# Kernel tuning notes

Measured on AMD Instinct MI355X. Metric: run time of the kernel, lower is better.

The kernel has to match this reference:

```python
import jax, jax.numpy as jnp
import numpy as np

BN_EPS = 1e-5


def spmm(rows, cols, vals, x):
    # Sparse [V,V] @ x for x: [B, V, F]. COO (rows, cols, vals) with E nnz.
    B, V, F = x.shape
    xt = jnp.transpose(x, (1, 0, 2)).reshape(V, B * F)      # [V, B*F]
    msg = xt[cols] * vals[:, None]                           # [E, B*F]
    y = jax.ops.segment_sum(msg, rows, num_segments=V)       # [V, B*F]
    return jnp.transpose(y.reshape(V, B, F), (1, 0, 2))      # [B, V, F]


def cheb_conv(rows, cols, vals, x, W, b):
    # Chebyshev graph conv: out = sum_k T_k(L) x @ W[k] + b ; W: [K, Fin, Fout]
    K = W.shape[0]
    x0 = x
    out = jnp.einsum('bvi,io->bvo', x0, W[0])
    if K > 1:
        x1 = spmm(rows, cols, vals, x0)
        out = out + jnp.einsum('bvi,io->bvo', x1, W[1])
        for k in range(2, K):
            x2 = 2.0 * spmm(rows, cols, vals, x1) - x0
            out = out + jnp.einsum('bvi,io->bvo', x2, W[k])
            x0, x1 = x1, x2
    return out + b


def bn_relu(x, gamma, beta):
    # BatchNorm1d (training stats) over (batch, nodes) per channel, then ReLU.
    m = jnp.mean(x, axis=(0, 1))
    v = jnp.var(x, axis=(0, 1))
    y = (x - m) * jax.lax.rsqrt(v + BN_EPS) * gamma + beta
    return jax.nn.relu(y)


def setup_inputs() -> dict:
    key = jax.random.key(0)
    ks = jax.random.split(key, 8)
    V, DEG, B, CIN, COUT = 49152, 20, 2, 128, 64
    x = jax.random.normal(ks[0], (B, V, CIN), dtype=jnp.float32)
    # HEALPix-like sparse Laplacian: diagonal + 20 random neighbors per node
    self_idx = jnp.arange(V, dtype=jnp.int32)
    nbr = jax.random.randint(ks[1], (V * DEG,), 0, V, dtype=jnp.int32)
    rows = jnp.concatenate([self_idx, jnp.repeat(self_idx, DEG)])
    cols = jnp.concatenate([self_idx, nbr])
    vals = jax.random.normal(ks[2], (V * (DEG + 1),), dtype=jnp.float32) * 0.1
    def w(k, shape):
        fan_in = shape[0] * shape[1]
        return jax.random.normal(k, shape, dtype=jnp.float32) * np.float32(np.sqrt(2.0 / fan_in))
    return {
        'x': x, 'rows': rows, 'cols': cols, 'vals': vals,
        'W1': w(ks[3], (1, CIN, COUT)), 'b1': jnp.zeros((COUT,), jnp.float32),
        'g1': jnp.ones((COUT,), jnp.float32), 'be1': jnp.zeros((COUT,), jnp.float32),
        'W2': w(ks[4], (3, COUT, COUT)), 'b2': jnp.zeros((COUT,), jnp.float32),
        'g2': jnp.ones((COUT,), jnp.float32), 'be2': jnp.zeros((COUT,), jnp.float32),
        'W3': w(ks[5], (1, COUT, CIN)), 'b3': jnp.zeros((CIN,), jnp.float32),
        'g3': jnp.ones((CIN,), jnp.float32), 'be3': jnp.zeros((CIN,), jnp.float32),
    }


def reference(x, rows, cols, vals, W1, b1, g1, be1, W2, b2, g2, be2, W3, b3, g3, be3):
    h = bn_relu(cheb_conv(rows, cols, vals, x, W1, b1), g1, be1)   # [B,V,64]
    h = bn_relu(cheb_conv(rows, cols, vals, h, W2, b2), g2, be2)   # [B,V,64]
    h = bn_relu(cheb_conv(rows, cols, vals, h, W3, b3), g3, be3)   # [B,V,128]
    return h
```

## Files before the change

### kernel.cpp

```cpp
#include <hip/hip_runtime.h>

#define VN 49152
#define DEG 20
#define NB 2
#define MROWS (NB * VN)

static constexpr float BN_EPS = 1e-5f;

typedef short bf16x8 __attribute__((ext_vector_type(8)));
typedef float floatx4 __attribute__((ext_vector_type(4)));

__device__ __forceinline__ unsigned short f2bf(float f) {
  unsigned int u = __builtin_bit_cast(unsigned int, f);
  u += 0x7FFFu + ((u >> 16) & 1u);
  return (unsigned short)(u >> 16);
}
__device__ __forceinline__ float bf2f(unsigned short h) {
  unsigned int u = ((unsigned int)h) << 16;
  return __builtin_bit_cast(float, u);
}
__device__ __forceinline__ float bflo(unsigned int u) {
  return __builtin_bit_cast(float, u << 16);
}
__device__ __forceinline__ float bfhi(unsigned int u) {
  return __builtin_bit_cast(float, u & 0xFFFF0000u);
}
__device__ __forceinline__ unsigned int packbf(float a, float b) {
  return (unsigned int)f2bf(a) | ((unsigned int)f2bf(b) << 16);
}


#define LDA1 136
__global__ __launch_bounds__(256) void gemm1(const float* __restrict__ X,
    const float* __restrict__ W, const float* __restrict__ bias,
    unsigned short* __restrict__ Y, float* __restrict__ st) {
  __shared__ unsigned short As[128 * LDA1];
  __shared__ unsigned short Bs[64 * LDA1];
  __shared__ float sred[128];
  int t = threadIdx.x;
  int row0 = blockIdx.x * 128;
  if (t < 128) sred[t] = 0.f;
  const float* Xt = X + (size_t)row0 * 128;
  #pragma unroll
  for (int c = 0; c < 16; ++c) {
    int f4i = c * 256 + t;
    int row = f4i >> 5, k = (f4i & 31) * 4;
    float4 v = *(const float4*)(Xt + row * 128 + k);
    *(uint2*)(&As[row * LDA1 + k]) = make_uint2(packbf(v.x, v.y), packbf(v.z, v.w));
  }
  #pragma unroll
  for (int c = 0; c < 32; ++c) {
    int f = c * 256 + t;
    int k = f >> 6, n = f & 63;
    Bs[n * LDA1 + k] = f2bf(W[f]);
  }
  __syncthreads();
  int l = t & 63, wv = t >> 6;
  int lr = l & 15, q = l >> 4;
  int m0 = wv * 32;
  floatx4 acc[2][4];
  #pragma unroll
  for (int mi = 0; mi < 2; ++mi)
    #pragma unroll
    for (int ni = 0; ni < 4; ++ni) acc[mi][ni] = (floatx4)(0.f);
  #pragma unroll
  for (int ks = 0; ks < 128; ks += 32) {
    bf16x8 af[2], bfr[4];
    #pragma unroll
    for (int mi = 0; mi < 2; ++mi)
      af[mi] = *(const bf16x8*)(&As[(m0 + mi * 16 + lr) * LDA1 + ks + q * 8]);
    #pragma unroll
    for (int ni = 0; ni < 4; ++ni)
      bfr[ni] = *(const bf16x8*)(&Bs[(ni * 16 + lr) * LDA1 + ks + q * 8]);
    #pragma unroll
    for (int mi = 0; mi < 2; ++mi)
      #pragma unroll
      for (int ni = 0; ni < 4; ++ni)
        acc[mi][ni] = __builtin_amdgcn_mfma_f32_16x16x32_bf16(af[mi], bfr[ni], acc[mi][ni], 0, 0, 0);
  }
  int b = (row0 >= VN) ? 1 : 0;
  int vbase = row0 - b * VN + m0;
  #pragma unroll
  for (int ni = 0; ni < 4; ++ni) {
    int col = ni * 16 + lr;
    float bv = bias[col];
    size_t sub = (size_t)(b * 2 + (col >> 5)) * VN;
    float s = 0.f, s2 = 0.f;
    #pragma unroll
    for (int mi = 0; mi < 2; ++mi)
      #pragma unroll
      for (int r = 0; r < 4; ++r) {
        float y = acc[mi][ni][r] + bv;
        s += y; s2 += y * y;
        int v = vbase + mi * 16 + q * 4 + r;
        Y[(sub + v) * 32 + (col & 31)] = f2bf(y);
      }
    atomicAdd(&sred[col], s);
    atomicAdd(&sred[64 + col], s2);
  }
  __syncthreads();
  if (t < 128) atomicAdd(&st[t], sred[t]);
}

#define LDA2 72
__global__ __launch_bounds__(256) void gemm2(const unsigned short* __restrict__ X0,
    const unsigned short* __restrict__ X1, const unsigned short* __restrict__ X2,
    const float* __restrict__ W, const float* __restrict__ bias,
    unsigned short* __restrict__ Y, float* __restrict__ st) {
  __shared__ unsigned short As[128 * LDA2];
  __shared__ unsigned short Bs[64 * LDA2];
  __shared__ float sred[128];
  int t = threadIdx.x;
  int row0 = blockIdx.x * 128;
  int b = (row0 >= VN) ? 1 : 0;
  int b2 = b * 2;
  int vb0 = row0 - b * VN;
  if (t < 128) sred[t] = 0.f;
  int l = t & 63, wv = t >> 6;
  int lr = l & 15, q = l >> 4;
  int m0 = wv * 32;
  floatx4 acc[2][4];
  #pragma unroll
  for (int mi = 0; mi < 2; ++mi)
    #pragma unroll
    for (int ni = 0; ni < 4; ++ni) acc[mi][ni] = (floatx4)(0.f);

  for (int term = 0; term < 3; ++term) {
    const unsigned short* Xp = (term == 0) ? X0 : (term == 1) ? X1 : X2;
    const float* Wt = W + term * 64 * 64;
    #pragma unroll
    for (int c8 = 0; c8 < 8; ++c8) {
      int i = c8 * 256 + t;
      int row = i >> 4, k = (i & 15) * 4;
      const unsigned short* src = Xp + ((size_t)(b2 + (k >> 5)) * VN + vb0 + row) * 32 + (k & 31);
      *(uint2*)(&As[row * LDA2 + k]) = *(const uint2*)src;
    }
    #pragma unroll
    for (int c = 0; c < 16; ++c) {
      int f = c * 256 + t;
      int k = f >> 6, n = f & 63;
      Bs[n * LDA2 + k] = f2bf(Wt[f]);
    }
    __syncthreads();
    #pragma unroll
    for (int ks = 0; ks < 64; ks += 32) {
      bf16x8 af[2], bfr[4];
      #pragma unroll
      for (int mi = 0; mi < 2; ++mi)
        af[mi] = *(const bf16x8*)(&As[(m0 + mi * 16 + lr) * LDA2 + ks + q * 8]);
      #pragma unroll
      for (int ni = 0; ni < 4; ++ni)
        bfr[ni] = *(const bf16x8*)(&Bs[(ni * 16 + lr) * LDA2 + ks + q * 8]);
      #pragma unroll
      for (int mi = 0; mi < 2; ++mi)
        #pragma unroll
        for (int ni = 0; ni < 4; ++ni)
          acc[mi][ni] = __builtin_amdgcn_mfma_f32_16x16x32_bf16(af[mi], bfr[ni], acc[mi][ni], 0, 0, 0);
    }
    __syncthreads();
  }
  int vbase = vb0 + m0;
  #pragma unroll
  for (int ni = 0; ni < 4; ++ni) {
    int col = ni * 16 + lr;
    float bv = bias[col];
    size_t sub = (size_t)(b2 + (col >> 5)) * VN;
    float s = 0.f, s2 = 0.f;
    #pragma unroll
    for (int mi = 0; mi < 2; ++mi)
      #pragma unroll
      for (int r = 0; r < 4; ++r) {
        float y = acc[mi][ni][r] + bv;
        s += y; s2 += y * y;
        int v = vbase + mi * 16 + q * 4 + r;
        Y[(sub + v) * 32 + (col & 31)] = f2bf(y);
      }
    atomicAdd(&sred[col], s);
    atomicAdd(&sred[64 + col], s2);
  }
  __syncthreads();
  if (t < 128) atomicAdd(&st[t], sred[t]);
}

__global__ __launch_bounds__(256) void gemm3(const unsigned short* __restrict__ X,
    const float* __restrict__ W, const float* __restrict__ bias,
    const float* __restrict__ st2, const float* __restrict__ gamma,
    const float* __restrict__ beta, unsigned short* __restrict__ Y,
    float* __restrict__ st3) {
  __shared__ unsigned short As[128 * LDA2];
  __shared__ unsigned short Bs[64 * LDA2];
  __shared__ float sred[128];
  __shared__ float scS[64], shS[64];
  int t = threadIdx.x;
  int row0 = blockIdx.x * 128;
  int n0 = blockIdx.y * 64;
  int b = (row0 >= VN) ? 1 : 0;
  int b2 = b * 2;
  int vb0 = row0 - b * VN;
  if (t < 128) sred[t] = 0.f;
  if (t < 64) {
    float mean = st2[t] * (1.f / MROWS);
    float var = st2[64 + t] * (1.f / MROWS) - mean * mean;
    float sc = gamma[t] * rsqrtf(var + BN_EPS);
    scS[t] = sc;
    shS[t] = beta[t] - mean * sc;
  }
  __syncthreads();
  #pragma unroll
  for (int c8 = 0; c8 < 8; ++c8) {
    int i = c8 * 256 + t;
    int row = i >> 4, k = (i & 15) * 4;
    const unsigned short* src = X + ((size_t)(b2 + (k >> 5)) * VN + vb0 + row) * 32 + (k & 31);
    uint2 rawv = *(const uint2*)src;
    float y0 = fmaf(bflo(rawv.x), scS[k + 0], shS[k + 0]);
    float y1 = fmaf(bfhi(rawv.x), scS[k + 1], shS[k + 1]);
    float y2 = fmaf(bflo(rawv.y), scS[k + 2], shS[k + 2]);
    float y3 = fmaf(bfhi(rawv.y), scS[k + 3], shS[k + 3]);
    y0 = y0 > 0.f ? y0 : 0.f; y1 = y1 > 0.f ? y1 : 0.f;
    y2 = y2 > 0.f ? y2 : 0.f; y3 = y3 > 0.f ? y3 : 0.f;
    *(uint2*)(&As[row * LDA2 + k]) = make_uint2(packbf(y0, y1), packbf(y2, y3));
  }
  #pragma unroll
  for (int c = 0; c < 16; ++c) {
    int f = c * 256 + t;
    int k = f >> 6, n = f & 63;
    Bs[n * LDA2 + k] = f2bf(W[k * 128 + n0 + n]);
  }
  __syncthreads();
  int l = t & 63, wv = t >> 6;
  int lr = l & 15, q = l >> 4;
  int m0 = wv * 32;
  floatx4 acc[2][4];
  #pragma unroll
  for (int mi = 0; mi < 2; ++mi)
    #pragma unroll
    for (int ni = 0; ni < 4; ++ni) acc[mi][ni] = (floatx4)(0.f);
  #pragma unroll
  for (int ks = 0; ks < 64; ks += 32) {
    bf16x8 af[2], bfr[4];
    #pragma unroll
    for (int mi = 0; mi < 2; ++mi)
      af[mi] = *(const bf16x8*)(&As[(m0 + mi * 16 + lr) * LDA2 + ks + q * 8]);
    #pragma unroll
    for (int ni = 0; ni < 4; ++ni)
      bfr[ni] = *(const bf16x8*)(&Bs[(ni * 16 + lr) * LDA2 + ks + q * 8]);
    #pragma unroll
    for (int mi = 0; mi < 2; ++mi)
      #pragma unroll
      for (int ni = 0; ni < 4; ++ni)
        acc[mi][ni] = __builtin_amdgcn_mfma_f32_16x16x32_bf16(af[mi], bfr[ni], acc[mi][ni], 0, 0, 0);
  }
  #pragma unroll
  for (int ni = 0; ni < 4; ++ni) {
    int lc = ni * 16 + lr;
    int col = n0 + lc;
    float bv = bias[col];
    float s = 0.f, s2 = 0.f;
    #pragma unroll
    for (int mi = 0; mi < 2; ++mi)
      #pragma unroll
      for (int r = 0; r < 4; ++r) {
        float y = acc[mi][ni][r] + bv;
        s += y; s2 += y * y;
        int row = row0 + m0 + mi * 16 + q * 4 + r;
        Y[(size_t)row * 128 + col] = f2bf(y);
      }
    atomicAdd(&sred[lc], s);
    atomicAdd(&sred[64 + lc], s2);
  }
  __syncthreads();
  if (t < 128) atomicAdd(&st3[n0 + ((t >> 6) << 7) + (t & 63)], sred[t]);
}

__global__ __launch_bounds__(256) void bn_h1(const unsigned short* __restrict__ T1,
    const float* __restrict__ st1, const float* __restrict__ gamma,
    const float* __restrict__ beta, unsigned short* __restrict__ H1) {
  __shared__ float scS[64], shS[64];
  int t = threadIdx.x;
  if (t < 64) {
    float mean = st1[t] * (1.f / MROWS);
    float var = st1[64 + t] * (1.f / MROWS) - mean * mean;
    float sc = gamma[t] * rsqrtf(var + BN_EPS);
    scS[t] = sc;
    shS[t] = beta[t] - mean * sc;
  }
  __syncthreads();
  int g = blockIdx.x;
  int combo = (g & 7) >> 1;
  int rg = ((g >> 3) << 1) | (g & 1);
  int wv = t >> 6, lane = t & 63;
  int v = rg * 64 + wv * 16 + (lane >> 2);
  int ch0 = (lane & 3) * 8;
  int cb = (combo & 1) * 32 + ch0;
  size_t off = (size_t)combo * VN * 32 + (size_t)v * 32 + ch0;
  uint4 d = *(const uint4*)(T1 + off);
  float y[8];
  y[0] = fmaf(bflo(d.x), scS[cb + 0], shS[cb + 0]);
  y[1] = fmaf(bfhi(d.x), scS[cb + 1], shS[cb + 1]);
  y[2] = fmaf(bflo(d.y), scS[cb + 2], shS[cb + 2]);
  y[3] = fmaf(bfhi(d.y), scS[cb + 3], shS[cb + 3]);
  y[4] = fmaf(bflo(d.z), scS[cb + 4], shS[cb + 4]);
  y[5] = fmaf(bfhi(d.z), scS[cb + 5], shS[cb + 5]);
  y[6] = fmaf(bflo(d.w), scS[cb + 6], shS[cb + 6]);
  y[7] = fmaf(bfhi(d.w), scS[cb + 7], shS[cb + 7]);
  #pragma unroll
  for (int j = 0; j < 8; ++j) y[j] = y[j] > 0.f ? y[j] : 0.f;
  uint4 o;
  o.x = packbf(y[0], y[1]); o.y = packbf(y[2], y[3]);
  o.z = packbf(y[4], y[5]); o.w = packbf(y[6], y[7]);
  *(uint4*)(H1 + off) = o;
}

__global__ __launch_bounds__(256) void spmm1(const unsigned short* __restrict__ H1,
    const int* __restrict__ cols, const float* __restrict__ vals,
    unsigned short* __restrict__ X1out) {
  int g = blockIdx.x;
  int combo = (g & 7) >> 1;
  int rg = ((g >> 3) << 1) | (g & 1);
  int t = threadIdx.x;
  int wv = t >> 6, lane = t & 63;
  int v = rg * 64 + wv * 16 + (lane >> 2);
  int ch0 = (lane & 3) * 8;
  const unsigned short* __restrict__ plane = H1 + (size_t)combo * VN * 32;
  int4  c4[5];
  float4 w4[5];
  const int4*   __restrict__ cp4 = (const int4*)(cols + VN + v * DEG);
  const float4* __restrict__ vp4 = (const float4*)(vals + VN + v * DEG);
  #pragma unroll
  for (int j = 0; j < 5; ++j) { c4[j] = cp4[j]; w4[j] = vp4[j]; }
  float a[8];
  {
    float w0 = vals[v];
    uint4 d = *(const uint4*)(plane + (size_t)v * 32 + ch0);
    a[0] = w0 * bflo(d.x); a[1] = w0 * bfhi(d.x);
    a[2] = w0 * bflo(d.y); a[3] = w0 * bfhi(d.y);
    a[4] = w0 * bflo(d.z); a[5] = w0 * bfhi(d.z);
    a[6] = w0 * bflo(d.w); a[7] = w0 * bfhi(d.w);
  }
  #pragma unroll
  for (int j = 0; j < 5; ++j) {
    const int cj[4] = {c4[j].x, c4[j].y, c4[j].z, c4[j].w};
    const float wj[4] = {w4[j].x, w4[j].y, w4[j].z, w4[j].w};
    #pragma unroll
    for (int e = 0; e < 4; ++e) {
      uint4 d = *(const uint4*)(plane + (size_t)cj[e] * 32 + ch0);
      float w = wj[e];
      a[0] = fmaf(bflo(d.x), w, a[0]); a[1] = fmaf(bfhi(d.x), w, a[1]);
      a[2] = fmaf(bflo(d.y), w, a[2]); a[3] = fmaf(bfhi(d.y), w, a[3]);
      a[4] = fmaf(bflo(d.z), w, a[4]); a[5] = fmaf(bfhi(d.z), w, a[5]);
      a[6] = fmaf(bflo(d.w), w, a[6]); a[7] = fmaf(bfhi(d.w), w, a[7]);
    }
  }
  uint4 o;
  o.x = packbf(a[0], a[1]); o.y = packbf(a[2], a[3]);
  o.z = packbf(a[4], a[5]); o.w = packbf(a[6], a[7]);
  *(uint4*)(X1out + (size_t)combo * VN * 32 + (size_t)v * 32 + ch0) = o;
}

__global__ __launch_bounds__(256) void spmm2(const unsigned short* __restrict__ X1,
    const unsigned short* __restrict__ H1, const int* __restrict__ cols,
    const float* __restrict__ vals, unsigned short* __restrict__ X2out) {
  int g = blockIdx.x;
  int combo = (g & 7) >> 1;
  int rg = ((g >> 3) << 1) | (g & 1);
  int t = threadIdx.x;
  int wv = t >> 6, lane = t & 63;
  int v = rg * 64 + wv * 16 + (lane >> 2);
  int ch0 = (lane & 3) * 8;
  const size_t pbase = (size_t)combo * VN * 32;
  const size_t myoff = pbase + (size_t)v * 32 + ch0;
  const unsigned short* __restrict__ plane = X1 + pbase;
  int4  c4[5];
  float4 w4[5];
  const int4*   __restrict__ cp4 = (const int4*)(cols + VN + v * DEG);
  const float4* __restrict__ vp4 = (const float4*)(vals + VN + v * DEG);
  #pragma unroll
  for (int j = 0; j < 5; ++j) { c4[j] = cp4[j]; w4[j] = vp4[j]; }
  float a[8];
  {
    float w0 = vals[v];
    uint4 d = *(const uint4*)(X1 + myoff);
    a[0] = w0 * bflo(d.x); a[1] = w0 * bfhi(d.x);
    a[2] = w0 * bflo(d.y); a[3] = w0 * bfhi(d.y);
    a[4] = w0 * bflo(d.z); a[5] = w0 * bfhi(d.z);
    a[6] = w0 * bflo(d.w); a[7] = w0 * bfhi(d.w);
  }
  #pragma unroll
  for (int j = 0; j < 5; ++j) {
    const int cj[4] = {c4[j].x, c4[j].y, c4[j].z, c4[j].w};
    const float wj[4] = {w4[j].x, w4[j].y, w4[j].z, w4[j].w};
    #pragma unroll
    for (int e = 0; e < 4; ++e) {
      uint4 d = *(const uint4*)(plane + (size_t)cj[e] * 32 + ch0);
      float w = wj[e];
      a[0] = fmaf(bflo(d.x), w, a[0]); a[1] = fmaf(bfhi(d.x), w, a[1]);
      a[2] = fmaf(bflo(d.y), w, a[2]); a[3] = fmaf(bfhi(d.y), w, a[3]);
      a[4] = fmaf(bflo(d.z), w, a[4]); a[5] = fmaf(bfhi(d.z), w, a[5]);
      a[6] = fmaf(bflo(d.w), w, a[6]); a[7] = fmaf(bfhi(d.w), w, a[7]);
    }
  }
  uint4 h = *(const uint4*)(H1 + myoff);
  uint4 o;
  o.x = packbf(2.f * a[0] - bflo(h.x), 2.f * a[1] - bfhi(h.x));
  o.y = packbf(2.f * a[2] - bflo(h.y), 2.f * a[3] - bfhi(h.y));
  o.z = packbf(2.f * a[4] - bflo(h.z), 2.f * a[5] - bfhi(h.z));
  o.w = packbf(2.f * a[6] - bflo(h.w), 2.f * a[7] - bfhi(h.w));
  *(uint4*)(X2out + myoff) = o;
}

__global__ __launch_bounds__(256) void bn_final(const unsigned short* __restrict__ T,
    float* __restrict__ Y, const float* __restrict__ st3,
    const float* __restrict__ gamma, const float* __restrict__ beta) {
  __shared__ float scS[128], shS[128];
  int t = threadIdx.x;
  if (t < 128) {
    float mean = st3[t] * (1.f / MROWS);
    float var = st3[128 + t] * (1.f / MROWS) - mean * mean;
    float sc = gamma[t] * rsqrtf(var + BN_EPS);
    scS[t] = sc;
    shS[t] = beta[t] - mean * sc;
  }
  __syncthreads();
  size_t i4 = ((size_t)blockIdx.x * 256 + t) * 4;
  int c0 = (int)(i4 & 127);
  ushort4 tv = *(const ushort4*)(T + i4);
  unsigned short sv[4] = {tv.x, tv.y, tv.z, tv.w};
  float ov[4];
  #pragma unroll
  for (int j = 0; j < 4; ++j) {
    int c = c0 + j;
    float y = fmaf(bf2f(sv[j]), scS[c], shS[c]);
    ov[j] = y > 0.f ? y : 0.f;
  }
  *(float4*)(Y + i4) = make_float4(ov[0], ov[1], ov[2], ov[3]);
}

extern "C" void kernel_launch(void* const* d_in, const int* in_sizes, int n_in,
                              void* d_out, int out_size, void* d_ws, size_t ws_size,
                              hipStream_t stream) {
  const float* x    = (const float*)d_in[0];
  const int*   cols = (const int*)  d_in[2];
  const float* vals = (const float*)d_in[3];
  const float* W1   = (const float*)d_in[4];
  const float* b1   = (const float*)d_in[5];
  const float* g1   = (const float*)d_in[6];
  const float* be1  = (const float*)d_in[7];
  const float* W2   = (const float*)d_in[8];
  const float* b2   = (const float*)d_in[9];
  const float* g2   = (const float*)d_in[10];
  const float* be2  = (const float*)d_in[11];
  const float* W3   = (const float*)d_in[12];
  const float* b3   = (const float*)d_in[13];
  const float* g3   = (const float*)d_in[14];
  const float* be3  = (const float*)d_in[15];
  float* out = (float*)d_out;

  const size_t PL = (size_t)MROWS * 64;
  unsigned short* P0 = (unsigned short*)d_ws;
  unsigned short* PH = P0 + PL;
  unsigned short* P1 = PH + PL;
  unsigned short* P2 = P1 + PL;
  float* st1 = (float*)(P2 + 2 * PL);
  float* st2 = st1 + 128;
  float* st3 = st2 + 128;

  hipMemsetAsync(st1, 0, 512 * sizeof(float), stream);

  dim3 blk(256);
  int rowb = MROWS / 128;
  int spmm_blocks = 3072;
  int ap128_blocks = (int)(PL * 2 / 4 / 256);

  gemm1<<<rowb, blk, 0, stream>>>(x, W1, b1, P0, st1);
  bn_h1<<<spmm_blocks, blk, 0, stream>>>(P0, st1, g1, be1, PH);

  spmm1<<<spmm_blocks, blk, 0, stream>>>(PH, cols, vals, P1);
  spmm2<<<spmm_blocks, blk, 0, stream>>>(P1, PH, cols, vals, P2);
  gemm2<<<rowb, blk, 0, stream>>>(PH, P1, P2, W2, b2, P0, st2);

  dim3 g3grid(rowb, 2);
  gemm3<<<g3grid, blk, 0, stream>>>(P0, W3, b3, st2, g2, be2, P2, st3);
  bn_final<<<ap128_blocks, blk, 0, stream>>>(P2, out, st3, g3, be3);
}
```

Measured before the change: 297.2 us.

## Fuse BN1 into SpMM gathers, fold second SpMM into gemm2, widen gemm3 tile

The standalone BN1+ReLU pass is removed. spmm1 now applies the batch-norm affine and ReLU on the fly to every gathered neighbour row, and gemm2 does the same for its T0 term. The second Chebyshev SpMM (2·L·x1 − x0) is computed inside gemm2 and written straight into the LDS A tile, so the X2 intermediate never goes to global memory. gemm3 now covers all 128 output columns in one block and stages its output in LDS so the global stores are coalesced uint4 writes. The goal is fewer kernel launches and less intermediate traffic, paid for with repeated BN arithmetic on each gather and with latency-bound gathers inside the GEMM kernel, which runs fewer threads per row.

```diff
diff --git a/kernel.cpp b/kernel.cpp
--- a/kernel.cpp
+++ b/kernel.cpp
@@ -27,6 +27,10 @@
 }
 __device__ __forceinline__ unsigned int packbf(float a, float b) {
   return (unsigned int)f2bf(a) | ((unsigned int)f2bf(b) << 16);
+}
+__device__ __forceinline__ void bfunpack8(const uint4& d, float* f) {
+  f[0] = bflo(d.x); f[1] = bfhi(d.x); f[2] = bflo(d.y); f[3] = bfhi(d.y);
+  f[4] = bflo(d.z); f[5] = bfhi(d.z); f[6] = bflo(d.w); f[7] = bfhi(d.w);
 }
 
 
@@ -102,20 +106,93 @@
   if (t < 128) atomicAdd(&st[t], sred[t]);
 }
 
+__global__ __launch_bounds__(256) void spmm1(const unsigned short* __restrict__ T1,
+    const int* __restrict__ cols, const float* __restrict__ vals,
+    const float* __restrict__ st1, const float* __restrict__ g1,
+    const float* __restrict__ be1, unsigned short* __restrict__ X1out) {
+  __shared__ float scS[64], shS[64];
+  int t = threadIdx.x;
+  if (t < 64) {
+    float mean = st1[t] * (1.f / MROWS);
+    float var = st1[64 + t] * (1.f / MROWS) - mean * mean;
+    float sc = g1[t] * rsqrtf(var + BN_EPS);
+    scS[t] = sc; shS[t] = be1[t] - mean * sc;
+  }
+  __syncthreads();
+  int g = blockIdx.x;
+  int combo = (g & 7) >> 1;
+  int rg = ((g >> 3) << 1) | (g & 1);
+  int wv = t >> 6, lane = t & 63;
+  int v = rg * 64 + wv * 16 + (lane >> 2);
+  int ch0 = (lane & 3) * 8;
+  int chg = (combo & 1) * 32 + ch0;
+  float sc8[8], sh8[8];
+  #pragma unroll
+  for (int j = 0; j < 8; ++j) { sc8[j] = scS[chg + j]; sh8[j] = shS[chg + j]; }
+  const unsigned short* __restrict__ plane = T1 + (size_t)combo * VN * 32;
+  int4  c4[5];
+  float4 w4[5];
+  const int4*   __restrict__ cp4 = (const int4*)(cols + VN + v * DEG);
+  const float4* __restrict__ vp4 = (const float4*)(vals + VN + v * DEG);
+  #pragma unroll
+  for (int j = 0; j < 5; ++j) { c4[j] = cp4[j]; w4[j] = vp4[j]; }
+  float a[8];
+  {
+    float w0 = vals[v];
+    uint4 d = *(const uint4*)(plane + (size_t)v * 32 + ch0);
+    float f[8]; bfunpack8(d, f);
+    #pragma unroll
+    for (int j = 0; j < 8; ++j) {
+      float h = fmaf(f[j], sc8[j], sh8[j]); h = h > 0.f ? h : 0.f;
+      a[j] = w0 * h;
+    }
+  }
+  #pragma unroll
+  for (int jj = 0; jj < 5; ++jj) {
+    const int cj[4] = {c4[jj].x, c4[jj].y, c4[jj].z, c4[jj].w};
+    const float wj[4] = {w4[jj].x, w4[jj].y, w4[jj].z, w4[jj].w};
+    #pragma unroll
+    for (int e = 0; e < 4; ++e) {
+      uint4 d = *(const uint4*)(plane + (size_t)cj[e] * 32 + ch0);
+      float f[8]; bfunpack8(d, f);
+      float w = wj[e];
+      #pragma unroll
+      for (int j = 0; j < 8; ++j) {
+        float h = fmaf(f[j], sc8[j], sh8[j]); h = h > 0.f ? h : 0.f;
+        a[j] = fmaf(h, w, a[j]);
+      }
+    }
+  }
+  uint4 o;
+  o.x = packbf(a[0], a[1]); o.y = packbf(a[2], a[3]);
+  o.z = packbf(a[4], a[5]); o.w = packbf(a[6], a[7]);
+  *(uint4*)(X1out + (size_t)combo * VN * 32 + (size_t)v * 32 + ch0) = o;
+}
+
 #define LDA2 72
-__global__ __launch_bounds__(256) void gemm2(const unsigned short* __restrict__ X0,
-    const unsigned short* __restrict__ X1, const unsigned short* __restrict__ X2,
+__global__ __launch_bounds__(256) void gemm2(const unsigned short* __restrict__ T1,
+    const unsigned short* __restrict__ X1, const int* __restrict__ cols,
+    const float* __restrict__ vals, const float* __restrict__ st1,
+    const float* __restrict__ g1, const float* __restrict__ be1,
     const float* __restrict__ W, const float* __restrict__ bias,
-    unsigned short* __restrict__ Y, float* __restrict__ st) {
+    unsigned short* __restrict__ Y, float* __restrict__ st2) {
   __shared__ unsigned short As[128 * LDA2];
   __shared__ unsigned short Bs[64 * LDA2];
   __shared__ float sred[128];
+  __shared__ float scS[64], shS[64];
   int t = threadIdx.x;
   int row0 = blockIdx.x * 128;
   int b = (row0 >= VN) ? 1 : 0;
   int b2 = b * 2;
   int vb0 = row0 - b * VN;
   if (t < 128) sred[t] = 0.f;
+  if (t < 64) {
+    float mean = st1[t] * (1.f / MROWS);
+    float var = st1[64 + t] * (1.f / MROWS) - mean * mean;
+    float sc = g1[t] * rsqrtf(var + BN_EPS);
+    scS[t] = sc; shS[t] = be1[t] - mean * sc;
+  }
+  __syncthreads();
   int l = t & 63, wv = t >> 6;
   int lr = l & 15, q = l >> 4;
   int m0 = wv * 32;
@@ -125,23 +202,15 @@
     #pragma unroll
     for (int ni = 0; ni < 4; ++ni) acc[mi][ni] = (floatx4)(0.f);
 
-  for (int term = 0; term < 3; ++term) {
-    const unsigned short* Xp = (term == 0) ? X0 : (term == 1) ? X1 : X2;
-    const float* Wt = W + term * 64 * 64;
-    #pragma unroll
-    for (int c8 = 0; c8 < 8; ++c8) {
-      int i = c8 * 256 + t;
-      int row = i >> 4, k = (i & 15) * 4;
-      const unsigned short* src = Xp + ((size_t)(b2 + (k >> 5)) * VN + vb0 + row) * 32 + (k & 31);
-      *(uint2*)(&As[row * LDA2 + k]) = *(const uint2*)src;
-    }
+  auto stage_b = [&](const float* Wt) {
     #pragma unroll
     for (int c = 0; c < 16; ++c) {
       int f = c * 256 + t;
       int k = f >> 6, n = f & 63;
       Bs[n * LDA2 + k] = f2bf(Wt[f]);
     }
-    __syncthreads();
+  };
+  auto mfma_tile = [&]() {
     #pragma unroll
     for (int ks = 0; ks < 64; ks += 32) {
       bf16x8 af[2], bfr[4];
@@ -157,8 +226,100 @@
         for (int ni = 0; ni < 4; ++ni)
           acc[mi][ni] = __builtin_amdgcn_mfma_f32_16x16x32_bf16(af[mi], bfr[ni], acc[mi][ni], 0, 0, 0);
     }
-    __syncthreads();
-  }
+  };
+
+  #pragma unroll 1
+  for (int it = 0; it < 4; ++it) {
+    int u = it * 256 + t;
+    int row = u >> 3;
+    int ch0 = (u & 7) * 8;
+    int hc = ch0 >> 5;
+    int cin = ch0 & 31;
+    int v = vb0 + row;
+    const unsigned short* __restrict__ pl = X1 + ((size_t)(b2 + hc) * VN) * 32 + cin;
+    const unsigned short* __restrict__ tp = T1 + ((size_t)(b2 + hc) * VN) * 32 + cin;
+    float sc8[8], sh8[8];
+    #pragma unroll
+    for (int j = 0; j < 8; ++j) { sc8[j] = scS[ch0 + j]; sh8[j] = shS[ch0 + j]; }
+    float h[8];
+    {
+      uint4 tv = *(const uint4*)(tp + (size_t)v * 32);
+      float f[8]; bfunpack8(tv, f);
+      #pragma unroll
+      for (int j = 0; j < 8; ++j) {
+        float y = fmaf(f[j], sc8[j], sh8[j]);
+        h[j] = y > 0.f ? y : 0.f;
+      }
+    }
+    float a[8];
+    {
+      float w0 = vals[v];
+      uint4 d = *(const uint4*)(pl + (size_t)v * 32);
+      float f[8]; bfunpack8(d, f);
+      #pragma unroll
+      for (int j = 0; j < 8; ++j) a[j] = w0 * f[j];
+    }
+    int4  c4[5];
+    float4 w4[5];
+    const int4*   __restrict__ cp4 = (const int4*)(cols + VN + v * DEG);
+    const float4* __restrict__ vp4 = (const float4*)(vals + VN + v * DEG);
+    #pragma unroll
+    for (int j = 0; j < 5; ++j) { c4[j] = cp4[j]; w4[j] = vp4[j]; }
+    #pragma unroll
+    for (int jj = 0; jj < 5; ++jj) {
+      const int cj[4] = {c4[jj].x, c4[jj].y, c4[jj].z, c4[jj].w};
+      const float wj[4] = {w4[jj].x, w4[jj].y, w4[jj].z, w4[jj].w};
+      #pragma unroll
+      for (int e = 0; e < 4; ++e) {
+        uint4 d = *(const uint4*)(pl + (size_t)cj[e] * 32);
+        float f[8]; bfunpack8(d, f);
+        float w = wj[e];
+        #pragma unroll
+        for (int j = 0; j < 8; ++j) a[j] = fmaf(f[j], w, a[j]);
+      }
+    }
+    uint4 o;
+    o.x = packbf(2.f * a[0] - h[0], 2.f * a[1] - h[1]);
+    o.y = packbf(2.f * a[2] - h[2], 2.f * a[3] - h[3]);
+    o.z = packbf(2.f * a[4] - h[4], 2.f * a[5] - h[5]);
+    o.w = packbf(2.f * a[6] - h[6], 2.f * a[7] - h[7]);
+    *(uint4*)(&As[row * LDA2 + ch0]) = o;
+  }
+  stage_b(W + 2 * 64 * 64);
+  __syncthreads();
+  mfma_tile();
+  __syncthreads();
+
+  #pragma unroll
+  for (int c8 = 0; c8 < 8; ++c8) {
+    int i = c8 * 256 + t;
+    int row = i >> 4, k = (i & 15) * 4;
+    const unsigned short* src = T1 + ((size_t)(b2 + (k >> 5)) * VN + vb0 + row) * 32 + (k & 31);
+    uint2 rawv = *(const uint2*)src;
+    float y0 = fmaf(bflo(rawv.x), scS[k + 0], shS[k + 0]);
+    float y1 = fmaf(bfhi(rawv.x), scS[k + 1], shS[k + 1]);
+    float y2 = fmaf(bflo(rawv.y), scS[k + 2], shS[k + 2]);
+    float y3 = fmaf(bfhi(rawv.y), scS[k + 3], shS[k + 3]);
+    y0 = y0 > 0.f ? y0 : 0.f; y1 = y1 > 0.f ? y1 : 0.f;
+    y2 = y2 > 0.f ? y2 : 0.f; y3 = y3 > 0.f ? y3 : 0.f;
+    *(uint2*)(&As[row * LDA2 + k]) = make_uint2(packbf(y0, y1), packbf(y2, y3));
+  }
+  stage_b(W);
+  __syncthreads();
+  mfma_tile();
+  __syncthreads();
+
+  #pragma unroll
+  for (int c8 = 0; c8 < 8; ++c8) {
+    int i = c8 * 256 + t;
+    int row = i >> 4, k = (i & 15) * 4;
+    const unsigned short* src = X1 + ((size_t)(b2 + (k >> 5)) * VN + vb0 + row) * 32 + (k & 31);
+    *(uint2*)(&As[row * LDA2 + k]) = *(const uint2*)src;
+  }
+  stage_b(W + 64 * 64);
+  __syncthreads();
+  mfma_tile();
+
   int vbase = vb0 + m0;
   #pragma unroll
   for (int ni = 0; ni < 4; ++ni) {
@@ -179,31 +340,31 @@
     atomicAdd(&sred[64 + col], s2);
   }
   __syncthreads();
-  if (t < 128) atomicAdd(&st[t], sred[t]);
-}
-
+  if (t < 128) atomicAdd(&st2[t], sred[t]);
+}
+
+#define LDC3 136
 __global__ __launch_bounds__(256) void gemm3(const unsigned short* __restrict__ X,
     const float* __restrict__ W, const float* __restrict__ bias,
     const float* __restrict__ st2, const float* __restrict__ gamma,
     const float* __restrict__ beta, unsigned short* __restrict__ Y,
     float* __restrict__ st3) {
-  __shared__ unsigned short As[128 * LDA2];
-  __shared__ unsigned short Bs[64 * LDA2];
-  __shared__ float sred[128];
+  __shared__ unsigned short smem[18432];
+  __shared__ float sred[256];
   __shared__ float scS[64], shS[64];
+  unsigned short* As = smem;
+  unsigned short* Bs = smem + 128 * LDA2;
   int t = threadIdx.x;
   int row0 = blockIdx.x * 128;
-  int n0 = blockIdx.y * 64;
   int b = (row0 >= VN) ? 1 : 0;
   int b2 = b * 2;
   int vb0 = row0 - b * VN;
-  if (t < 128) sred[t] = 0.f;
+  sred[t] = 0.f;
   if (t < 64) {
     float mean = st2[t] * (1.f / MROWS);
     float var = st2[64 + t] * (1.f / MROWS) - mean * mean;
     float sc = gamma[t] * rsqrtf(var + BN_EPS);
-    scS[t] = sc;
-    shS[t] = beta[t] - mean * sc;
+    scS[t] = sc; shS[t] = beta[t] - mean * sc;
   }
   __syncthreads();
   #pragma unroll
@@ -221,39 +382,40 @@
     *(uint2*)(&As[row * LDA2 + k]) = make_uint2(packbf(y0, y1), packbf(y2, y3));
   }
   #pragma unroll
-  for (int c = 0; c < 16; ++c) {
+  for (int c = 0; c < 32; ++c) {
     int f = c * 256 + t;
-    int k = f >> 6, n = f & 63;
-    Bs[n * LDA2 + k] = f2bf(W[k * 128 + n0 + n]);
+    int k = f >> 7, n = f & 127;
+    Bs[n * LDA2 + k] = f2bf(W[k * 128 + n]);
   }
   __syncthreads();
   int l = t & 63, wv = t >> 6;
   int lr = l & 15, q = l >> 4;
   int m0 = wv * 32;
-  floatx4 acc[2][4];
+  floatx4 acc[2][8];
   #pragma unroll
   for (int mi = 0; mi < 2; ++mi)
     #pragma unroll
-    for (int ni = 0; ni < 4; ++ni) acc[mi][ni] = (floatx4)(0.f);
+    for (int ni = 0; ni < 8; ++ni) acc[mi][ni] = (floatx4)(0.f);
   #pragma unroll
   for (int ks = 0; ks < 64; ks += 32) {
-    bf16x8 af[2], bfr[4];
+    bf16x8 af[2], bfr[8];
     #pragma unroll
     for (int mi = 0; mi < 2; ++mi)
       af[mi] = *(const bf16x8*)(&As[(m0 + mi * 16 + lr) * LDA2 + ks + q * 8]);
     #pragma unroll
-    for (int ni = 0; ni < 4; ++ni)
+    for (int ni = 0; ni < 8; ++ni)
       bfr[ni] = *(const bf16x8*)(&Bs[(ni * 16 + lr) * LDA2 + ks + q * 8]);
     #pragma unroll
     for (int mi = 0; mi < 2; ++mi)
       #pragma unroll
-      for (int ni = 0; ni < 4; ++ni)
+      for (int ni = 0; ni < 8; ++ni)
         acc[mi][ni] = __builtin_amdgcn_mfma_f32_16x16x32_bf16(af[mi], bfr[ni], acc[mi][ni], 0, 0, 0);
   }
-  #pragma unroll
-  for (int ni = 0; ni < 4; ++ni) {
-    int lc = ni * 16 + lr;
-    int col = n0 + lc;
+  __syncthreads();
+  unsigned short* OutS = smem;
+  #pragma unroll
+  for (int ni = 0; ni < 8; ++ni) {
+    int col = ni * 16 + lr;
     float bv = bias[col];
     float s = 0.f, s2 = 0.f;
     #pragma unroll
@@ -262,150 +424,21 @@
       for (int r = 0; r < 4; ++r) {
         float y = acc[mi][ni][r] + bv;
         s += y; s2 += y * y;
-        int row = row0 + m0 + mi * 16 + q * 4 + r;
-        Y[(size_t)row * 128 + col] = f2bf(y);
+        int row = m0 + mi * 16 + q * 4 + r;
+        OutS[row * LDC3 + col] = f2bf(y);
       }
-    atomicAdd(&sred[lc], s);
-    atomicAdd(&sred[64 + lc], s2);
-  }
-  __syncthreads();
-  if (t < 128) atomicAdd(&st3[n0 + ((t >> 6) << 7) + (t & 63)], sred[t]);
-}
-
-__global__ __launch_bounds__(256) void bn_h1(const unsigned short* __restrict__ T1,
-    const float* __restrict__ st1, const float* __restrict__ gamma,
-    const float* __restrict__ beta, unsigned short* __restrict__ H1) {
-  __shared__ float scS[64], shS[64];
-  int t = threadIdx.x;
-  if (t < 64) {
-    float mean = st1[t] * (1.f / MROWS);
-    float var = st1[64 + t] * (1.f / MROWS) - mean * mean;
-    float sc = gamma[t] * rsqrtf(var + BN_EPS);
-    scS[t] = sc;
-    shS[t] = beta[t] - mean * sc;
-  }
-  __syncthreads();
-  int g = blockIdx.x;
-  int combo = (g & 7) >> 1;
-  int rg = ((g >> 3) << 1) | (g & 1);
-  int wv = t >> 6, lane = t & 63;
-  int v = rg * 64 + wv * 16 + (lane >> 2);
-  int ch0 = (lane & 3) * 8;
-  int cb = (combo & 1) * 32 + ch0;
-  size_t off = (size_t)combo * VN * 32 + (size_t)v * 32 + ch0;
-  uint4 d = *(const uint4*)(T1 + off);
-  float y[8];
-  y[0] = fmaf(bflo(d.x), scS[cb + 0], shS[cb + 0]);
-  y[1] = fmaf(bfhi(d.x), scS[cb + 1], shS[cb + 1]);
-  y[2] = fmaf(bflo(d.y), scS[cb + 2], shS[cb + 2]);
-  y[3] = fmaf(bfhi(d.y), scS[cb + 3], shS[cb + 3]);
-  y[4] = fmaf(bflo(d.z), scS[cb + 4], shS[cb + 4]);
-  y[5] = fmaf(bfhi(d.z), scS[cb + 5], shS[cb + 5]);
-  y[6] = fmaf(bflo(d.w), scS[cb + 6], shS[cb + 6]);
-  y[7] = fmaf(bfhi(d.w), scS[cb + 7], shS[cb + 7]);
-  #pragma unroll
-  for (int j = 0; j < 8; ++j) y[j] = y[j] > 0.f ? y[j] : 0.f;
-  uint4 o;
-  o.x = packbf(y[0], y[1]); o.y = packbf(y[2], y[3]);
-  o.z = packbf(y[4], y[5]); o.w = packbf(y[6], y[7]);
-  *(uint4*)(H1 + off) = o;
-}
-
-__global__ __launch_bounds__(256) void spmm1(const unsigned short* __restrict__ H1,
-    const int* __restrict__ cols, const float* __restrict__ vals,
-    unsigned short* __restrict__ X1out) {
-  int g = blockIdx.x;
-  int combo = (g & 7) >> 1;
-  int rg = ((g >> 3) << 1) | (g & 1);
-  int t = threadIdx.x;
-  int wv = t >> 6, lane = t & 63;
-  int v = rg * 64 + wv * 16 + (lane >> 2);
-  int ch0 = (lane & 3) * 8;
-  const unsigned short* __restrict__ plane = H1 + (size_t)combo * VN * 32;
-  int4  c4[5];
-  float4 w4[5];
-  const int4*   __restrict__ cp4 = (const int4*)(cols + VN + v * DEG);
-  const float4* __restrict__ vp4 = (const float4*)(vals + VN + v * DEG);
-  #pragma unroll
-  for (int j = 0; j < 5; ++j) { c4[j] = cp4[j]; w4[j] = vp4[j]; }
-  float a[8];
-  {
-    float w0 = vals[v];
-    uint4 d = *(const uint4*)(plane + (size_t)v * 32 + ch0);
-    a[0] = w0 * bflo(d.x); a[1] = w0 * bfhi(d.x);
-    a[2] = w0 * bflo(d.y); a[3] = w0 * bfhi(d.y);
-    a[4] = w0 * bflo(d.z); a[5] = w0 * bfhi(d.z);
-    a[6] = w0 * bflo(d.w); a[7] = w0 * bfhi(d.w);
-  }
-  #pragma unroll
-  for (int j = 0; j < 5; ++j) {
-    const int cj[4] = {c4[j].x, c4[j].y, c4[j].z, c4[j].w};
-    const float wj[4] = {w4[j].x, w4[j].y, w4[j].z, w4[j].w};
-    #pragma unroll
-    for (int e = 0; e < 4; ++e) {
-      uint4 d = *(const uint4*)(plane + (size_t)cj[e] * 32 + ch0);
-      float w = wj[e];
-      a[0] = fmaf(bflo(d.x), w, a[0]); a[1] = fmaf(bfhi(d.x), w, a[1]);
-      a[2] = fmaf(bflo(d.y), w, a[2]); a[3] = fmaf(bfhi(d.y), w, a[3]);
-      a[4] = fmaf(bflo(d.z), w, a[4]); a[5] = fmaf(bfhi(d.z), w, a[5]);
-      a[6] = fmaf(bflo(d.w), w, a[6]); a[7] = fmaf(bfhi(d.w), w, a[7]);
-    }
-  }
-  uint4 o;
-  o.x = packbf(a[0], a[1]); o.y = packbf(a[2], a[3]);
-  o.z = packbf(a[4], a[5]); o.w = packbf(a[6], a[7]);
-  *(uint4*)(X1out + (size_t)combo * VN * 32 + (size_t)v * 32 + ch0) = o;
-}
-
-__global__ __launch_bounds__(256) void spmm2(const unsigned short* __restrict__ X1,
-    const unsigned short* __restrict__ H1, const int* __restrict__ cols,
-    const float* __restrict__ vals, unsigned short* __restrict__ X2out) {
-  int g = blockIdx.x;
-  int combo = (g & 7) >> 1;
-  int rg = ((g >> 3) << 1) | (g & 1);
-  int t = threadIdx.x;
-  int wv = t >> 6, lane = t & 63;
-  int v = rg * 64 + wv * 16 + (lane >> 2);
-  int ch0 = (lane & 3) * 8;
-  const size_t pbase = (size_t)combo * VN * 32;
-  const size_t myoff = pbase + (size_t)v * 32 + ch0;
-  const unsigned short* __restrict__ plane = X1 + pbase;
-  int4  c4[5];
-  float4 w4[5];
-  const int4*   __restrict__ cp4 = (const int4*)(cols + VN + v * DEG);
-  const float4* __restrict__ vp4 = (const float4*)(vals + VN + v * DEG);
-  #pragma unroll
-  for (int j = 0; j < 5; ++j) { c4[j] = cp4[j]; w4[j] = vp4[j]; }
-  float a[8];
-  {
-    float w0 = vals[v];
-    uint4 d = *(const uint4*)(X1 + myoff);
-    a[0] = w0 * bflo(d.x); a[1] = w0 * bfhi(d.x);
-    a[2] = w0 * bflo(d.y); a[3] = w0 * bfhi(d.y);
-    a[4] = w0 * bflo(d.z); a[5] = w0 * bfhi(d.z);
-    a[6] = w0 * bflo(d.w); a[7] = w0 * bfhi(d.w);
-  }
-  #pragma unroll
-  for (int j = 0; j < 5; ++j) {
-    const int cj[4] = {c4[j].x, c4[j].y, c4[j].z, c4[j].w};
-    const float wj[4] = {w4[j].x, w4[j].y, w4[j].z, w4[j].w};
-    #pragma unroll
-    for (int e = 0; e < 4; ++e) {
-      uint4 d = *(const uint4*)(plane + (size_t)cj[e] * 32 + ch0);
-      float w = wj[e];
-      a[0] = fmaf(bflo(d.x), w, a[0]); a[1] = fmaf(bfhi(d.x), w, a[1]);
-      a[2] = fmaf(bflo(d.y), w, a[2]); a[3] = fmaf(bfhi(d.y), w, a[3]);
-      a[4] = fmaf(bflo(d.z), w, a[4]); a[5] = fmaf(bfhi(d.z), w, a[5]);
-      a[6] = fmaf(bflo(d.w), w, a[6]); a[7] = fmaf(bfhi(d.w), w, a[7]);
-    }
-  }
-  uint4 h = *(const uint4*)(H1 + myoff);
-  uint4 o;
-  o.x = packbf(2.f * a[0] - bflo(h.x), 2.f * a[1] - bfhi(h.x));
-  o.y = packbf(2.f * a[2] - bflo(h.y), 2.f * a[3] - bfhi(h.y));
-  o.z = packbf(2.f * a[4] - bflo(h.z), 2.f * a[5] - bfhi(h.z));
-  o.w = packbf(2.f * a[6] - bflo(h.w), 2.f * a[7] - bfhi(h.w));
-  *(uint4*)(X2out + myoff) = o;
+    atomicAdd(&sred[col], s);
+    atomicAdd(&sred[128 + col], s2);
+  }
+  __syncthreads();
+  atomicAdd(&st3[t], sred[t]);
+  #pragma unroll
+  for (int c = 0; c < 8; ++c) {
+    int idx = c * 256 + t;
+    int row = idx >> 4, seg = idx & 15;
+    *(uint4*)(Y + ((size_t)(row0 + row)) * 128 + seg * 8) =
+        *(const uint4*)(&OutS[row * LDC3 + seg * 8]);
+  }
 }
 
 __global__ __launch_bounds__(256) void bn_final(const unsigned short* __restrict__ T,
@@ -457,8 +490,7 @@
 
   const size_t PL = (size_t)MROWS * 64;
   unsigned short* P0 = (unsigned short*)d_ws;
-  unsigned short* PH = P0 + PL;
-  unsigned short* P1 = PH + PL;
+  unsigned short* P1 = P0 + PL;
   unsigned short* P2 = P1 + PL;
   float* st1 = (float*)(P2 + 2 * PL);
   float* st2 = st1 + 128;
@@ -472,13 +504,11 @@
   int ap128_blocks = (int)(PL * 2 / 4 / 256);
 
   gemm1<<<rowb, blk, 0, stream>>>(x, W1, b1, P0, st1);
-  bn_h1<<<spmm_blocks, blk, 0, stream>>>(P0, st1, g1, be1, PH);
-
-  spmm1<<<spmm_blocks, blk, 0, stream>>>(PH, cols, vals, P1);
-  spmm2<<<spmm_blocks, blk, 0, stream>>>(P1, PH, cols, vals, P2);
-  gemm2<<<rowb, blk, 0, stream>>>(PH, P1, P2, W2, b2, P0, st2);
-
-  dim3 g3grid(rowb, 2);
-  gemm3<<<g3grid, blk, 0, stream>>>(P0, W3, b3, st2, g2, be2, P2, st3);
+
+  spmm1<<<spmm_blocks, blk, 0, stream>>>(P0, cols, vals, st1, g1, be1, P1);
+  gemm2<<<rowb, blk, 0, stream>>>(P0, P1, cols, vals, st1, g1, be1,
+                                  W2, b2, P0, st2);
+
+  gemm3<<<rowb, blk, 0, stream>>>(P0, W3, b3, st2, g2, be2, P2, st3);
   bn_final<<<ap128_blocks, blk, 0, stream>>>(P2, out, st3, g3, be3);
 }
```

Result: slower. 327.8 us (+10.3%).
